# Kernel tuning notes

Hardware: AMD Instinct MI355X
Metric: run time of the kernel (lower is better)

## Reference

```python
import jax, jax.numpy as jnp
import numpy as np

N_PE = 100000   # num 'pe' nodes
N_R = 100000    # num 'router' nodes
E = 600000      # edges per relation
D_IN = 64       # input feature dim per node type
H = 128         # hidden_channels
G = 64          # graphs in batch


def setup_inputs() -> dict:
    key = jax.random.key(0)
    ks = jax.random.split(key, 20)
    inp = {}
    inp["x_pe"] = jax.random.normal(ks[0], (N_PE, D_IN), jnp.float32)
    inp["x_r"] = jax.random.normal(ks[1], (N_R, D_IN), jnp.float32)
    # edge_index per relation: row0 = src node ids, row1 = dst node ids
    inp["ei_per"] = jax.random.randint(ks[2], (2, E), 0, N_PE, jnp.int32)   # pe -> router
    inp["ei_rpe"] = jax.random.randint(ks[3], (2, E), 0, N_R, jnp.int32)    # router -> pe
    inp["ei_rr"] = jax.random.randint(ks[4], (2, E), 0, N_R, jnp.int32)     # router -> router
    inp["batch_pe"] = jnp.sort(jax.random.randint(ks[5], (N_PE,), 0, G, jnp.int32))
    inp["batch_r"] = jnp.sort(jax.random.randint(ks[6], (N_R,), 0, G, jnp.int32))
    # GraphConv params, relation axis ordered [pe->router, router->pe, router->router]
    s1 = 1.0 / np.sqrt(D_IN)
    s2 = 1.0 / np.sqrt(H)
    inp["Wrel1"] = jax.random.normal(ks[7], (3, D_IN, H), jnp.float32) * s1
    inp["brel1"] = jnp.zeros((3, H), jnp.float32)
    inp["Wroot1"] = jax.random.normal(ks[8], (3, D_IN, H), jnp.float32) * s1
    inp["Wrel23"] = jax.random.normal(ks[9], (2, 3, H, H), jnp.float32) * s2
    inp["brel23"] = jnp.zeros((2, 3, H), jnp.float32)
    inp["Wroot23"] = jax.random.normal(ks[10], (2, 3, H, H), jnp.float32) * s2
    # per-node-type MLP heads, type axis ordered [pe, router]
    inp["mlp_W1"] = jax.random.normal(ks[11], (2, H, 5), jnp.float32) * s2
    inp["mlp_b1"] = jnp.zeros((2, 5), jnp.float32)
    inp["mlp_W2"] = jax.random.normal(ks[12], (2, 5, 1), jnp.float32) * (1.0 / np.sqrt(5.0))
    inp["mlp_b2"] = jnp.zeros((2, 1), jnp.float32)
    inp["out_W"] = jax.random.normal(ks[13], (2, 1), jnp.float32) * (1.0 / np.sqrt(2.0))
    inp["out_b"] = jnp.zeros((1,), jnp.float32)
    return inp


def _hetero_graphconv(x_pe, x_r, ei_per, ei_rpe, ei_rr, Wrel, brel, Wroot):
    # GraphConv: lin_rel(scatter_add(x_src)) + lin_root(x_dst); to_hetero sums per dst type.
    agg_r_from_pe = jax.ops.segment_sum(x_pe[ei_per[0]], ei_per[1], num_segments=N_R)
    agg_pe_from_r = jax.ops.segment_sum(x_r[ei_rpe[0]], ei_rpe[1], num_segments=N_PE)
    agg_r_from_r = jax.ops.segment_sum(x_r[ei_rr[0]], ei_rr[1], num_segments=N_R)
    o_pe = agg_pe_from_r @ Wrel[1] + brel[1] + x_pe @ Wroot[1]
    o_r = (agg_r_from_pe @ Wrel[0] + brel[0] + x_r @ Wroot[0]) \
        + (agg_r_from_r @ Wrel[2] + brel[2] + x_r @ Wroot[2])
    return o_pe, o_r


def reference(x_pe, x_r, ei_per, ei_rpe, ei_rr, batch_pe, batch_r,
              Wrel1, brel1, Wroot1, Wrel23, brel23, Wroot23,
              mlp_W1, mlp_b1, mlp_W2, mlp_b2, out_W, out_b):
    h_pe, h_r = _hetero_graphconv(x_pe, x_r, ei_per, ei_rpe, ei_rr, Wrel1, brel1, Wroot1)
    h_pe, h_r = jax.nn.relu(h_pe), jax.nn.relu(h_r)
    h_pe, h_r = _hetero_graphconv(h_pe, h_r, ei_per, ei_rpe, ei_rr, Wrel23[0], brel23[0], Wroot23[0])
    h_pe, h_r = jax.nn.relu(h_pe), jax.nn.relu(h_r)
    h_pe, h_r = _hetero_graphconv(h_pe, h_r, ei_per, ei_rpe, ei_rr, Wrel23[1], brel23[1], Wroot23[1])
    gm_pe = jax.ops.segment_max(h_pe, batch_pe, num_segments=G)  # [G, H]
    gm_r = jax.ops.segment_max(h_r, batch_r, num_segments=G)
    def mlp(x, W1, b1, W2, b2):
        return jax.nn.relu(x @ W1 + b1) @ W2 + b2
    o_pe = mlp(gm_pe, mlp_W1[0], mlp_b1[0], mlp_W2[0], mlp_b2[0])  # [G, 1]
    o_r = mlp(gm_r, mlp_W1[1], mlp_b1[1], mlp_W2[1], mlp_b2[1])
    cat = jnp.concatenate([o_pe, o_r], axis=1)  # [G, 2]
    return cat @ out_W + out_b  # [G, 1]
```

## Files before the change

### kernel.cpp

```cpp
#include <hip/hip_runtime.h>
#include <cstddef>
#include <cstdint>

#define DIN 64
#define HID 128
#define NBKMAX 256
#define EPB 2048

typedef _Float16 half4v __attribute__((ext_vector_type(4)));
typedef _Float16 half8v __attribute__((ext_vector_type(8)));
typedef float f32x16 __attribute__((ext_vector_type(16)));

__device__ __forceinline__ unsigned encf(float f) {
    unsigned b = __float_as_uint(f);
    return (b & 0x80000000u) ? ~b : (b | 0x80000000u);
}
__device__ __forceinline__ float decf(unsigned u) {
    unsigned b = (u & 0x80000000u) ? (u & 0x7FFFFFFFu) : ~u;
    return __uint_as_float(b);
}

__global__ void conv_x2_k(const float* s0, _Float16* d0, int n40,
                          const float* s1, _Float16* d1, int n41) {
    int r = blockIdx.y;
    const float* s = r == 0 ? s0 : s1;
    _Float16* d = r == 0 ? d0 : d1;
    int n4 = r == 0 ? n40 : n41;
    int i = blockIdx.x * 256 + threadIdx.x;
    if (i >= n4) return;
    float4 v = *reinterpret_cast<const float4*>(&s[i * 4]);
    half4v h;
    h.x = (_Float16)v.x; h.y = (_Float16)v.y; h.z = (_Float16)v.z; h.w = (_Float16)v.w;
    *reinterpret_cast<half4v*>(&d[i * 4]) = h;
}

struct CW { const float* src; const float* src2; _Float16* dst; int K; int total; };
__global__ __launch_bounds__(256) void prep_k(
    CW c0, CW c1, CW c2, CW c3, CW c4, CW c5, CW c6, CW c7,
    const int* e0, const int* e1, const int* e2, int E,
    int* hc0, int* hc1, int* hc2,
    const int* bpe, int npe, int* spe,
    const int* brr, int nrr, int* srr, int G) {
    int y = blockIdx.y;
    if (y < 8) {
        CW J;
        switch (y) {
            case 0: J = c0; break; case 1: J = c1; break; case 2: J = c2; break;
            case 3: J = c3; break; case 4: J = c4; break; case 5: J = c5; break;
            case 6: J = c6; break; default: J = c7; break;
        }
        int i = blockIdx.x * 256 + threadIdx.x;
        if (i >= J.total) return;
        int m = i / (J.K * HID);
        int rem = i % (J.K * HID);
        int k = rem / HID;
        int col = rem % HID;
        float v = J.src[i];
        if (J.src2) v += J.src2[i];
        J.dst[(size_t)m * HID * J.K + (size_t)col * J.K + k] = (_Float16)v;
    } else if (y < 11) {
        int r = y - 8;
        const int* ei = r == 0 ? e0 : (r == 1 ? e1 : e2);
        int* cnt = r == 0 ? hc0 : (r == 1 ? hc1 : hc2);
        __shared__ int sc[NBKMAX];
        int t = threadIdx.x;
        sc[t] = 0;
        __syncthreads();
        int base = blockIdx.x * EPB;
        if (base >= E) return;
        int n = min(EPB, E - base);
        for (int i = t; i < n; i += 256)
            atomicAdd(&sc[(unsigned)ei[E + base + i] >> 9], 1);
        __syncthreads();
        if (sc[t]) atomicAdd(&cnt[t], sc[t]);
    } else {
        int r = blockIdx.x;
        if (r >= 2) return;
        const int* batch = r == 0 ? bpe : brr;
        int n = r == 0 ? npe : nrr;
        int* starts = r == 0 ? spe : srr;
        int g = threadIdx.x;
        if (g > G) return;
        int lo = 0, hi = n;
        while (lo < hi) {
            int mid = (lo + hi) >> 1;
            if (batch[mid] < g) lo = mid + 1; else hi = mid;
        }
        starts[g] = lo;
    }
}

__global__ __launch_bounds__(256) void bscan_k(int* c0, int* bb0, int* cu0, int* rp0, int n0,
                                               int* c1, int* bb1, int* cu1, int* rp1, int n1,
                                               int* c2, int* bb2, int* cu2, int* rp2, int n2,
                                               int E) {
    __shared__ int sh[256];
    int t = threadIdx.x;
    for (int r = 0; r < 3; ++r) {
        int* cnt = r == 0 ? c0 : (r == 1 ? c1 : c2);
        int* bb  = r == 0 ? bb0 : (r == 1 ? bb1 : bb2);
        int* cu  = r == 0 ? cu0 : (r == 1 ? cu1 : cu2);
        int* rp  = r == 0 ? rp0 : (r == 1 ? rp1 : rp2);
        int N    = r == 0 ? n0 : (r == 1 ? n1 : n2);
        int v = cnt[t];
        sh[t] = v;
        __syncthreads();
        for (int off = 1; off < 256; off <<= 1) {
            int val = (t >= off) ? sh[t - off] : 0;
            __syncthreads();
            sh[t] += val;
            __syncthreads();
        }
        int ex = sh[t] - v;
        bb[t] = ex;
        cu[t] = ex;
        if (t == 255) bb[256] = sh[255];
        if (t == 0) rp[N] = E;
        __syncthreads();
    }
}

__global__ __launch_bounds__(256) void bin_k(const int* e0, const int* e1, const int* e2, int E,
                                             int* cu0, int* cu1, int* cu2,
                                             unsigned* t0, unsigned* t1, unsigned* t2) {
    int r = blockIdx.y;
    const int* ei = r == 0 ? e0 : (r == 1 ? e1 : e2);
    int* gcur = r == 0 ? cu0 : (r == 1 ? cu1 : cu2);
    unsigned* temp = r == 0 ? t0 : (r == 1 ? t1 : t2);
    __shared__ unsigned pk[EPB];
    __shared__ unsigned short bkb[EPB];
    __shared__ int cnt[NBKMAX];
    __shared__ int scn[NBKMAX];
    __shared__ int rb[NBKMAX];
    int t = threadIdx.x;
    int base = blockIdx.x * EPB;
    int n = min(EPB, E - base);
    cnt[t] = 0;
    __syncthreads();
    for (int i = t; i < n; i += 256)
        atomicAdd(&cnt[(unsigned)ei[E + base + i] >> 9], 1);
    __syncthreads();
    {
        int v = cnt[t];
        scn[t] = v;
        __syncthreads();
        for (int off = 1; off < 256; off <<= 1) {
            int val = (t >= off) ? scn[t - off] : 0;
            __syncthreads();
            scn[t] += val;
            __syncthreads();
        }
        int ex = scn[t] - v;
        __syncthreads();
        scn[t] = ex;
    }
    {
        int c = cnt[t];
        rb[t] = c ? atomicAdd(&gcur[t], c) : 0;
        cnt[t] = 0;
    }
    __syncthreads();
    for (int i = t; i < n; i += 256) {
        int s = ei[base + i];
        int d = ei[E + base + i];
        int b = (unsigned)d >> 9;
        int slot = scn[b] + atomicAdd(&cnt[b], 1);
        pk[slot] = ((unsigned)s << 9) | (unsigned)(d & 511);
        bkb[slot] = (unsigned short)b;
    }
    __syncthreads();
    for (int i = t; i < n; i += 256) {
        int b = bkb[i];
        temp[rb[b] + (i - scn[b])] = pk[i];
    }
}

__global__ __launch_bounds__(256) void bcsr_k(const unsigned* t0, const unsigned* t1, const unsigned* t2,
                                              const int* bb0, const int* bb1, const int* bb2,
                                              int* rp0, int* rp1, int* rp2,
                                              int* a0, int* a1, int* a2,
                                              int n0, int n1, int n2) {
    int r = blockIdx.y;
    const unsigned* temp = r == 0 ? t0 : (r == 1 ? t1 : t2);
    const int* bb = r == 0 ? bb0 : (r == 1 ? bb1 : bb2);
    int* rp = r == 0 ? rp0 : (r == 1 ? rp1 : rp2);
    int* adj = r == 0 ? a0 : (r == 1 ? a1 : a2);
    int N = r == 0 ? n0 : (r == 1 ? n1 : n2);
    int b = blockIdx.x;
    int lo = bb[b], hi = bb[b + 1];
    __shared__ int cnt[512];
    __shared__ int sh[256];
    int t = threadIdx.x;
    cnt[t] = 0; cnt[t + 256] = 0;
    __syncthreads();
    for (int i = lo + t; i < hi; i += 256)
        atomicAdd(&cnt[temp[i] & 511], 1);
    __syncthreads();
    int c0 = cnt[2 * t], c1 = cnt[2 * t + 1];
    sh[t] = c0 + c1;
    __syncthreads();
    for (int off = 1; off < 256; off <<= 1) {
        int v = (t >= off) ? sh[t - off] : 0;
        __syncthreads();
        sh[t] += v;
        __syncthreads();
    }
    int pairExcl = sh[t] - (c0 + c1);
    __syncthreads();
    int e0x = lo + pairExcl;
    int e1x = e0x + c0;
    cnt[2 * t] = e0x;
    cnt[2 * t + 1] = e1x;
    int nodeBase = b * 512;
    if (nodeBase + 2 * t < N) rp[nodeBase + 2 * t] = e0x;
    if (nodeBase + 2 * t + 1 < N) rp[nodeBase + 2 * t + 1] = e1x;
    __syncthreads();
    for (int i = lo + t; i < hi; i += 256) {
        unsigned p = temp[i];
        int pos = atomicAdd(&cnt[p & 511], 1);
        adj[pos] = p >> 9;
    }
}

struct AJob { const _Float16* X; const int* rp; const int* adj; _Float16* AGG; int N; int gb; };
template <int D>
__global__ __launch_bounds__(256) void gather3_k(AJob a0, AJob a1, AJob a2) {
    int b = blockIdx.x;
    AJob J;
    if (b < a0.gb) { J = a0; }
    else if (b < a0.gb + a1.gb) { J = a1; b -= a0.gb; }
    else { J = a2; b -= a0.gb + a1.gb; }
    constexpr int TPN = D / 8;
    constexpr int NPB = 256 / TPN;
    int node = b * NPB + threadIdx.x / TPN;
    int glane = threadIdx.x % TPN;
    if (node >= J.N) return;
    int a = J.rp[node], e1 = J.rp[node + 1];
    float acc[8] = {0.f, 0.f, 0.f, 0.f, 0.f, 0.f, 0.f, 0.f};
    for (int base = a; base < e1; base += TPN) {
        int idx = base + glane;
        int myAdj = (idx < e1) ? J.adj[idx] : 0;
        int cnt = min(TPN, e1 - base);
        int j = 0;
        for (; j + 4 <= cnt; j += 4) {
            int s0 = __shfl(myAdj, j, TPN);
            int s1 = __shfl(myAdj, j + 1, TPN);
            int s2 = __shfl(myAdj, j + 2, TPN);
            int s3 = __shfl(myAdj, j + 3, TPN);
            half8v v0 = *reinterpret_cast<const half8v*>(&J.X[(size_t)s0 * D + glane * 8]);
            half8v v1 = *reinterpret_cast<const half8v*>(&J.X[(size_t)s1 * D + glane * 8]);
            half8v v2 = *reinterpret_cast<const half8v*>(&J.X[(size_t)s2 * D + glane * 8]);
            half8v v3 = *reinterpret_cast<const half8v*>(&J.X[(size_t)s3 * D + glane * 8]);
#pragma unroll
            for (int i = 0; i < 8; ++i)
                acc[i] += (float)v0[i] + (float)v1[i] + (float)v2[i] + (float)v3[i];
        }
        for (; j < cnt; ++j) {
            int s0 = __shfl(myAdj, j, TPN);
            half8v v0 = *reinterpret_cast<const half8v*>(&J.X[(size_t)s0 * D + glane * 8]);
#pragma unroll
            for (int i = 0; i < 8; ++i) acc[i] += (float)v0[i];
        }
    }
    half8v o;
#pragma unroll
    for (int i = 0; i < 8; ++i) o[i] = (_Float16)acc[i];
    *reinterpret_cast<half8v*>(&J.AGG[(size_t)node * D + glane * 8]) = o;
}

struct GJob {
    const _Float16* A0; const _Float16* A1; const _Float16* A2;
    const _Float16* W0; const _Float16* W1; const _Float16* W2;
    const float* b0; const float* b1;
    _Float16* O;
    int N; int total; int gb;
};

template <bool RELU>
__global__ __launch_bounds__(256) void gemm2_k(GJob j0, GJob j1, int K, int lg) {
    const bool second = ((int)blockIdx.x >= j0.gb);
    const GJob J = second ? j1 : j0;
    const int bx = blockIdx.x - (second ? j0.gb : 0);
    __shared__ _Float16 Alds[128 * 64];
    __shared__ _Float16 Wlds[128 * 64];
    const int tid = threadIdx.x;
    const int lane = tid & 63;
    const int w = tid >> 6;
    const int wr = w & 1, wc = w >> 1;
    const int rowBase = bx * 128;

    f32x16 acc[2][2];
#pragma unroll
    for (int r = 0; r < 2; ++r)
#pragma unroll
        for (int c = 0; c < 2; ++c)
#pragma unroll
            for (int q = 0; q < 16; ++q) acc[r][c][q] = 0.0f;

    const _Float16* Ap[3] = {J.A0, J.A1, J.A2};

    const int row = tid & 127;
    const int kh = (tid >> 7) * 32;
    const int gr = rowBase + row;
    const bool rowOK = (gr < J.N);
    int offS[4];
#pragma unroll
    for (int j = 0; j < 4; ++j) {
        int t = (kh >> 4) + (j >> 1);
        int k8 = j & 1;
        offS[j] = (((row >> 5) * 4 + t) * 64 + (row & 31) + 32 * k8) * 8;
    }

    const int total = J.total;
    const int cmask = (1 << lg) - 1;

    auto ldA = [&](int c, half8v h[4]) {
        int s = c >> lg;
        int k0 = (c & cmask) * 64;
        half8v z = {};
        h[0] = z; h[1] = z; h[2] = z; h[3] = z;
        if (rowOK) {
            const _Float16* p = Ap[s] + (size_t)gr * K + k0 + kh;
#pragma unroll
            for (int j = 0; j < 4; ++j) h[j] = *reinterpret_cast<const half8v*>(p + j * 8);
        }
    };
    auto ldW = [&](int c, half8v h[4]) {
        int s = c >> lg;
        int k0 = (c & cmask) * 64;
        const _Float16* __restrict__ Wt = (s == 0) ? J.W0 : (s == 1 ? J.W1 : J.W2);
        const _Float16* p = Wt + (size_t)row * K + k0 + kh;
#pragma unroll
        for (int j = 0; j < 4; ++j) h[j] = *reinterpret_cast<const half8v*>(p + j * 8);
    };

    half8v ra[4], rw[4];
    ldA(0, ra); ldW(0, rw);
#pragma unroll
    for (int j = 0; j < 4; ++j) {
        *reinterpret_cast<half8v*>(&Alds[offS[j]]) = ra[j];
        *reinterpret_cast<half8v*>(&Wlds[offS[j]]) = rw[j];
    }
    __syncthreads();

    for (int c = 0; c < total; ++c) {
        const bool more = (c + 1 < total);
        if (more) { ldA(c + 1, ra); ldW(c + 1, rw); }
#pragma unroll
        for (int t = 0; t < 4; ++t) {
            half8v av[2], wv[2];
#pragma unroll
            for (int r = 0; r < 2; ++r)
                av[r] = *reinterpret_cast<const half8v*>(&Alds[(((wr * 2 + r) * 4 + t) * 64 + lane) * 8]);
#pragma unroll
            for (int cc = 0; cc < 2; ++cc)
                wv[cc] = *reinterpret_cast<const half8v*>(&Wlds[(((wc * 2 + cc) * 4 + t) * 64 + lane) * 8]);
#pragma unroll
            for (int r = 0; r < 2; ++r)
#pragma unroll
                for (int cc = 0; cc < 2; ++cc)
                    acc[r][cc] = __builtin_amdgcn_mfma_f32_32x32x16_f16(wv[cc], av[r], acc[r][cc], 0, 0, 0);
        }
        __syncthreads();
        if (more) {
#pragma unroll
            for (int j = 0; j < 4; ++j) {
                *reinterpret_cast<half8v*>(&Alds[offS[j]]) = ra[j];
                *reinterpret_cast<half8v*>(&Wlds[offS[j]]) = rw[j];
            }
            __syncthreads();
        }
    }

    const int half_ = lane >> 5;
#pragma unroll
    for (int r = 0; r < 2; ++r) {
        int node = rowBase + (wr * 2 + r) * 32 + (lane & 31);
        bool ok = (node < J.N);
        _Float16* orow = J.O + (size_t)node * HID;
#pragma unroll
        for (int cc = 0; cc < 2; ++cc) {
            int fbase = wc * 64 + cc * 32;
#pragma unroll
            for (int g = 0; g < 4; ++g) {
                int fmine = fbase + g * 8 + 4 * half_;
                float4 bv = *reinterpret_cast<const float4*>(&J.b0[fmine]);
                if (J.b1) {
                    float4 b2v = *reinterpret_cast<const float4*>(&J.b1[fmine]);
                    bv.x += b2v.x; bv.y += b2v.y; bv.z += b2v.z; bv.w += b2v.w;
                }
                union { half4v h; int i[2]; } m, p;
#pragma unroll
                for (int i = 0; i < 4; ++i) {
                    float v = acc[r][cc][g * 4 + i] + ((const float*)&bv)[i];
                    if (RELU) v = fmaxf(v, 0.f);
                    m.h[i] = (_Float16)v;
                }
                p.i[0] = __shfl_xor(m.i[0], 32);
                p.i[1] = __shfl_xor(m.i[1], 32);
                half4v lo = half_ ? p.h : m.h;
                half4v hi = half_ ? m.h : p.h;
                half8v outv;
#pragma unroll
                for (int i = 0; i < 4; ++i) { outv[i] = lo[i]; outv[4 + i] = hi[i]; }
                if (ok && ((g & 1) == half_))
                    *reinterpret_cast<half8v*>(&orow[fbase + g * 8]) = outv;
            }
        }
    }
}

__global__ __launch_bounds__(128) void seg_max2_k(const _Float16* H0, const int* st0, unsigned* g0,
                                                  const _Float16* H1, const int* st1, unsigned* g1) {
    int z = blockIdx.z;
    const _Float16* Hf = z == 0 ? H0 : H1;
    const int* starts = z == 0 ? st0 : st1;
    unsigned* gmU = z == 0 ? g0 : g1;
    int g = blockIdx.x;
    int sub = blockIdx.y;
    int SUB = gridDim.y;
    int f = threadIdx.x;
    int s0 = starts[g], s1 = starts[g + 1];
    int len = s1 - s0;
    if (len <= 0) return;
    int chunk = (len + SUB - 1) / SUB;
    int a = s0 + sub * chunk;
    int b = min(a + chunk, s1);
    if (a >= b) return;
    float m = -__builtin_huge_valf();
    for (int n = a; n < b; ++n) m = fmaxf(m, (float)Hf[(size_t)n * HID + f]);
    atomicMax(&gmU[g * HID + f], encf(m));
}

__global__ void head_k(const unsigned* __restrict__ gmU_pe, const unsigned* __restrict__ gmU_r,
                       const float* __restrict__ W1, const float* __restrict__ b1,
                       const float* __restrict__ W2, const float* __restrict__ b2,
                       const float* __restrict__ oW, const float* __restrict__ ob,
                       float* __restrict__ out, int G) {
    int g = threadIdx.x;
    if (g >= G) return;
    float vals[2];
#pragma unroll
    for (int t = 0; t < 2; ++t) {
        const unsigned* gm = t ? gmU_r : gmU_pe;
        float z[5];
#pragma unroll
        for (int j = 0; j < 5; ++j) z[j] = b1[t * 5 + j];
        for (int f = 0; f < HID; ++f) {
            float x = decf(gm[g * HID + f]);
#pragma unroll
            for (int j = 0; j < 5; ++j) z[j] = fmaf(x, W1[t * HID * 5 + f * 5 + j], z[j]);
        }
        float o = b2[t];
#pragma unroll
        for (int j = 0; j < 5; ++j) o = fmaf(fmaxf(z[j], 0.f), W2[t * 5 + j], o);
        vals[t] = o;
    }
    out[g] = vals[0] * oW[0] + vals[1] * oW[1] + ob[0];
}

extern "C" void kernel_launch(void* const* d_in, const int* in_sizes, int n_in,
                              void* d_out, int out_size, void* d_ws, size_t ws_size,
                              hipStream_t stream) {
    const float* x_pe    = (const float*)d_in[0];
    const float* x_r     = (const float*)d_in[1];
    const int* ei_per    = (const int*)d_in[2];
    const int* ei_rpe    = (const int*)d_in[3];
    const int* ei_rr     = (const int*)d_in[4];
    const int* batch_pe  = (const int*)d_in[5];
    const int* batch_r   = (const int*)d_in[6];
    const float* Wrel1   = (const float*)d_in[7];
    const float* brel1   = (const float*)d_in[8];
    const float* Wroot1  = (const float*)d_in[9];
    const float* Wrel23  = (const float*)d_in[10];
    const float* brel23  = (const float*)d_in[11];
    const float* Wroot23 = (const float*)d_in[12];
    const float* mlp_W1  = (const float*)d_in[13];
    const float* mlp_b1  = (const float*)d_in[14];
    const float* mlp_W2  = (const float*)d_in[15];
    const float* mlp_b2  = (const float*)d_in[16];
    const float* out_W   = (const float*)d_in[17];
    const float* out_b   = (const float*)d_in[18];
    float* out = (float*)d_out;

    const int N_PE = in_sizes[0] / DIN;
    const int N_R  = in_sizes[1] / DIN;
    const int E    = in_sizes[2] / 2;
    const int G    = out_size;
    const int NMAX = (N_PE > N_R) ? N_PE : N_R;
    const size_t SZM = (size_t)NMAX * HID;

    _Float16* H1 = (_Float16*)d_ws;
    _Float16* H2 = H1 + SZM;
    _Float16* H3 = H2 + SZM;
    _Float16* H4 = H3 + SZM;
    _Float16* H5 = H4 + SZM;
    _Float16* xh_pe = H5 + SZM;
    _Float16* xh_r  = xh_pe + (size_t)N_PE * DIN;
    _Float16* wt_rel1    = xh_r + (size_t)N_R * DIN;
    _Float16* wt_root1pe = wt_rel1 + 3 * DIN * HID;
    _Float16* wt_wsum1   = wt_root1pe + DIN * HID;
    _Float16* wt_rel23   = wt_wsum1 + DIN * HID;
    _Float16* wt_root_l2 = wt_rel23 + 6 * HID * HID;
    _Float16* wt_root_l3 = wt_root_l2 + HID * HID;
    _Float16* wt_wsum2   = wt_root_l3 + HID * HID;
    _Float16* wt_wsum3   = wt_wsum2 + HID * HID;
    unsigned* gmU_pe = (unsigned*)(wt_wsum3 + HID * HID);
    unsigned* gmU_r  = gmU_pe + G * HID;
    int* bktCnt = (int*)(gmU_r + G * HID);
    int* starts_pe = bktCnt + 3 * NBKMAX;
    int* starts_r  = starts_pe + (G + 1);
    int* bb     = starts_r + (G + 1);
    int* gcur   = bb + 3 * (NBKMAX + 1);
    int* csr    = gcur + 3 * NBKMAX;
    const size_t relstride = (size_t)(NMAX + 1) + 2 * (size_t)E + 16;

    int* rp[3]; int* adjp[3]; unsigned* tmp[3];
    const int Nds[3] = {N_R, N_PE, N_R};
    for (int r = 0; r < 3; ++r) {
        int* rowptr = csr + (size_t)r * relstride;
        rp[r] = rowptr;
        adjp[r] = rowptr + (Nds[r] + 1);
        tmp[r] = (unsigned*)(adjp[r] + E);
    }

    const int gpe = (N_PE + 127) / 128, grr = (N_R + 127) / 128;
    const int eb = (E + EPB - 1) / EPB;

    hipMemsetAsync(gmU_pe, 0, (2 * (size_t)G * HID + 3 * NBKMAX) * sizeof(int), stream);
    {
        int n40 = N_PE * DIN / 4, n41 = N_R * DIN / 4;
        int nmax = n40 > n41 ? n40 : n41;
        dim3 g((nmax + 255) / 256, 2);
        conv_x2_k<<<g, 256, 0, stream>>>(x_pe, xh_pe, n40, x_r, xh_r, n41);
    }
    {
        CW c0{Wrel1, nullptr, wt_rel1, DIN, 3 * DIN * HID};
        CW c1{Wroot1 + 1 * DIN * HID, nullptr, wt_root1pe, DIN, DIN * HID};
        CW c2{Wroot1, Wroot1 + 2 * DIN * HID, wt_wsum1, DIN, DIN * HID};
        CW c3{Wrel23, nullptr, wt_rel23, HID, 6 * HID * HID};
        CW c4{Wroot23 + 1 * HID * HID, nullptr, wt_root_l2, HID, HID * HID};
        CW c5{Wroot23 + 4 * HID * HID, nullptr, wt_root_l3, HID, HID * HID};
        CW c6{Wroot23, Wroot23 + 2 * HID * HID, wt_wsum2, HID, HID * HID};
        CW c7{Wroot23 + 3 * HID * HID, Wroot23 + 5 * HID * HID, wt_wsum3, HID, HID * HID};
        int gx = (6 * HID * HID + 255) / 256;
        if (eb > gx) gx = eb;
        dim3 g(gx, 12);
        prep_k<<<g, 256, 0, stream>>>(c0, c1, c2, c3, c4, c5, c6, c7,
                                      ei_per, ei_rpe, ei_rr, E,
                                      bktCnt, bktCnt + NBKMAX, bktCnt + 2 * NBKMAX,
                                      batch_pe, N_PE, starts_pe,
                                      batch_r, N_R, starts_r, G);
    }
    {
        bscan_k<<<1, 256, 0, stream>>>(
            bktCnt, bb, gcur, rp[0], Nds[0],
            bktCnt + NBKMAX, bb + (NBKMAX + 1), gcur + NBKMAX, rp[1], Nds[1],
            bktCnt + 2 * NBKMAX, bb + 2 * (NBKMAX + 1), gcur + 2 * NBKMAX, rp[2], Nds[2], E);
        dim3 gh(eb, 3);
        bin_k<<<gh, 256, 0, stream>>>(ei_per, ei_rpe, ei_rr, E,
                                      gcur, gcur + NBKMAX, gcur + 2 * NBKMAX,
                                      tmp[0], tmp[1], tmp[2]);
        dim3 gc(NBKMAX, 3);
        bcsr_k<<<gc, 256, 0, stream>>>(tmp[0], tmp[1], tmp[2],
                                       bb, bb + (NBKMAX + 1), bb + 2 * (NBKMAX + 1),
                                       rp[0], rp[1], rp[2],
                                       adjp[0], adjp[1], adjp[2],
                                       Nds[0], Nds[1], Nds[2]);
    }

    {
        AJob a0{xh_r, rp[1], adjp[1], H1, N_PE, (N_PE + 31) / 32};
        AJob a1{xh_pe, rp[0], adjp[0], H2, N_R, (N_R + 31) / 32};
        AJob a2{xh_r, rp[2], adjp[2], H3, N_R, (N_R + 31) / 32};
        gather3_k<DIN><<<a0.gb + a1.gb + a2.gb, 256, 0, stream>>>(a0, a1, a2);
        GJob jp{H1, xh_pe, nullptr,
                wt_rel1 + 1 * DIN * HID, wt_root1pe, nullptr,
                brel1 + HID, nullptr, H4, N_PE, 2, gpe};
        GJob jr{H2, H3, xh_r,
                wt_rel1, wt_rel1 + 2 * DIN * HID, wt_wsum1,
                brel1, brel1 + 2 * HID, H5, N_R, 3, grr};
        gemm2_k<true><<<gpe + grr, 256, 0, stream>>>(jp, jr, DIN, 0);
    }
    {
        AJob a0{H5, rp[1], adjp[1], H1, N_PE, (N_PE + 15) / 16};
        AJob a1{H4, rp[0], adjp[0], H2, N_R, (N_R + 15) / 16};
        AJob a2{H5, rp[2], adjp[2], H3, N_R, (N_R + 15) / 16};
        gather3_k<HID><<<a0.gb + a1.gb + a2.gb, 256, 0, stream>>>(a0, a1, a2);
        GJob jp{H1, H4, nullptr,
                wt_rel23 + 1 * HID * HID, wt_root_l2, nullptr,
                brel23 + HID, nullptr, H1, N_PE, 2 * 2, gpe};
        GJob jr{H2, H3, H5,
                wt_rel23, wt_rel23 + 2 * HID * HID, wt_wsum2,
                brel23, brel23 + 2 * HID, H2, N_R, 3 * 2, grr};
        gemm2_k<true><<<gpe + grr, 256, 0, stream>>>(jp, jr, HID, 1);
    }
    {
        AJob a0{H2, rp[1], adjp[1], H3, N_PE, (N_PE + 15) / 16};
        AJob a1{H1, rp[0], adjp[0], H4, N_R, (N_R + 15) / 16};
        AJob a2{H2, rp[2], adjp[2], H5, N_R, (N_R + 15) / 16};
        gather3_k<HID><<<a0.gb + a1.gb + a2.gb, 256, 0, stream>>>(a0, a1, a2);
        GJob jp{H3, H1, nullptr,
                wt_rel23 + 4 * HID * HID, wt_root_l3, nullptr,
                brel23 + 4 * HID, nullptr, H3, N_PE, 2 * 2, gpe};
        GJob jr{H4, H5, H2,
                wt_rel23 + 3 * HID * HID, wt_rel23 + 5 * HID * HID, wt_wsum3,
                brel23 + 3 * HID, brel23 + 5 * HID, H4, N_R, 3 * 2, grr};
        gemm2_k<false><<<gpe + grr, 256, 0, stream>>>(jp, jr, HID, 1);
    }

    dim3 gs(G, 16, 2);
    seg_max2_k<<<gs, 128, 0, stream>>>(H3, starts_pe, gmU_pe, H4, starts_r, gmU_r);
    head_k<<<1, 64, 0, stream>>>(gmU_pe, gmU_r, mlp_W1, mlp_b1, mlp_W2, mlp_b2, out_W, out_b, out, G);
}
```

Measured before the change: 590.0 us.

## Double-buffer GEMM tiles via direct global-to-LDS loads with XOR swizzle

Rewrites the staging of the fused dual-job GEMM kernel. Tiles now go straight from global memory into LDS with global_load_lds instead of passing through registers, and the LDS buffers are doubled so the next K-chunk loads while the current one feeds MFMA. Each chunk ends with a single waitcnt+barrier instead of two syncthreads. An XOR swizzle on the 16-byte column groups is meant to avoid LDS bank conflicts on the fragment reads. The per-row bounds check on A is dropped, so the last partial row block may read past N unless the buffers are padded. LDS use also doubles, which may reduce occupancy.

New measurement: 547.9 us. 1.08x faster.

```diff
diff --git a/kernel.cpp b/kernel.cpp
--- a/kernel.cpp
+++ b/kernel.cpp
@@ -281,8 +281,8 @@
     const bool second = ((int)blockIdx.x >= j0.gb);
     const GJob J = second ? j1 : j0;
     const int bx = blockIdx.x - (second ? j0.gb : 0);
-    __shared__ _Float16 Alds[128 * 64];
-    __shared__ _Float16 Wlds[128 * 64];
+    __shared__ _Float16 Alds[2][128 * 64];
+    __shared__ _Float16 Wlds[2][128 * 64];
     const int tid = threadIdx.x;
     const int lane = tid & 63;
     const int w = tid >> 6;
@@ -298,78 +298,74 @@
             for (int q = 0; q < 16; ++q) acc[r][c][q] = 0.0f;
 
     const _Float16* Ap[3] = {J.A0, J.A1, J.A2};
-
-    const int row = tid & 127;
-    const int kh = (tid >> 7) * 32;
-    const int gr = rowBase + row;
-    const bool rowOK = (gr < J.N);
-    int offS[4];
-#pragma unroll
-    for (int j = 0; j < 4; ++j) {
-        int t = (kh >> 4) + (j >> 1);
-        int k8 = j & 1;
-        offS[j] = (((row >> 5) * 4 + t) * 64 + (row & 31) + 32 * k8) * 8;
+    const _Float16* Wp[3] = {J.W0, J.W1, J.W2};
+
+    int srow[4];
+    int soff[4];
+    int ldsoff[4];
+#pragma unroll
+    for (int i = 0; i < 4; ++i) {
+        int r_ = (w * 4 + i) * 8 + (lane >> 3);
+        srow[i] = r_;
+        soff[i] = ((lane & 7) ^ (r_ & 7)) << 4;
+        ldsoff[i] = (w * 4 + i) << 10;
     }
 
     const int total = J.total;
     const int cmask = (1 << lg) - 1;
 
-    auto ldA = [&](int c, half8v h[4]) {
-        int s = c >> lg;
-        int k0 = (c & cmask) * 64;
-        half8v z = {};
-        h[0] = z; h[1] = z; h[2] = z; h[3] = z;
-        if (rowOK) {
-            const _Float16* p = Ap[s] + (size_t)gr * K + k0 + kh;
-#pragma unroll
-            for (int j = 0; j < 4; ++j) h[j] = *reinterpret_cast<const half8v*>(p + j * 8);
+    auto stage = [&](int c, int buf) {
+        const int s = c >> lg;
+        const int k0b = (c & cmask) << 7;
+        const char* Ab = (const char*)Ap[s];
+        const char* Wb = (const char*)Wp[s];
+        char* al = (char*)&Alds[buf][0];
+        char* wl = (char*)&Wlds[buf][0];
+#pragma unroll
+        for (int i = 0; i < 4; ++i) {
+            const char* ga = Ab + ((size_t)(rowBase + srow[i]) * K) * 2 + k0b + soff[i];
+            const char* gw = Wb + ((size_t)srow[i] * K) * 2 + k0b + soff[i];
+            __builtin_amdgcn_global_load_lds(
+                (const __attribute__((address_space(1))) void*)ga,
+                (__attribute__((address_space(3))) void*)(al + ldsoff[i]), 16, 0, 0);
+            __builtin_amdgcn_global_load_lds(
+                (const __attribute__((address_space(1))) void*)gw,
+                (__attribute__((address_space(3))) void*)(wl + ldsoff[i]), 16, 0, 0);
         }
     };
-    auto ldW = [&](int c, half8v h[4]) {
-        int s = c >> lg;
-        int k0 = (c & cmask) * 64;
-        const _Float16* __restrict__ Wt = (s == 0) ? J.W0 : (s == 1 ? J.W1 : J.W2);
-        const _Float16* p = Wt + (size_t)row * K + k0 + kh;
-#pragma unroll
-        for (int j = 0; j < 4; ++j) h[j] = *reinterpret_cast<const half8v*>(p + j * 8);
-    };
-
-    half8v ra[4], rw[4];
-    ldA(0, ra); ldW(0, rw);
-#pragma unroll
-    for (int j = 0; j < 4; ++j) {
-        *reinterpret_cast<half8v*>(&Alds[offS[j]]) = ra[j];
-        *reinterpret_cast<half8v*>(&Wlds[offS[j]]) = rw[j];
-    }
-    __syncthreads();
+
+    stage(0, 0);
+    asm volatile("s_waitcnt vmcnt(0)\n\ts_barrier" ::: "memory");
+
+    const int rA0 = wr * 64 + (lane & 31);
+    const int cW0 = wc * 64 + (lane & 31);
+    const int ghi = lane >> 5;
 
     for (int c = 0; c < total; ++c) {
-        const bool more = (c + 1 < total);
-        if (more) { ldA(c + 1, ra); ldW(c + 1, rw); }
+        if (c + 1 < total) stage(c + 1, (c + 1) & 1);
+        const _Float16* al = &Alds[c & 1][0];
+        const _Float16* wl = &Wlds[c & 1][0];
 #pragma unroll
         for (int t = 0; t < 4; ++t) {
+            const int g = 2 * t + ghi;
             half8v av[2], wv[2];
 #pragma unroll
-            for (int r = 0; r < 2; ++r)
-                av[r] = *reinterpret_cast<const half8v*>(&Alds[(((wr * 2 + r) * 4 + t) * 64 + lane) * 8]);
-#pragma unroll
-            for (int cc = 0; cc < 2; ++cc)
-                wv[cc] = *reinterpret_cast<const half8v*>(&Wlds[(((wc * 2 + cc) * 4 + t) * 64 + lane) * 8]);
+            for (int r = 0; r < 2; ++r) {
+                const int row = rA0 + r * 32;
+                av[r] = *reinterpret_cast<const half8v*>(al + ((row * 8 + (g ^ (row & 7))) << 3));
+            }
+#pragma unroll
+            for (int cc = 0; cc < 2; ++cc) {
+                const int col = cW0 + cc * 32;
+                wv[cc] = *reinterpret_cast<const half8v*>(wl + ((col * 8 + (g ^ (col & 7))) << 3));
+            }
 #pragma unroll
             for (int r = 0; r < 2; ++r)
 #pragma unroll
                 for (int cc = 0; cc < 2; ++cc)
                     acc[r][cc] = __builtin_amdgcn_mfma_f32_32x32x16_f16(wv[cc], av[r], acc[r][cc], 0, 0, 0);
         }
-        __syncthreads();
-        if (more) {
-#pragma unroll
-            for (int j = 0; j < 4; ++j) {
-                *reinterpret_cast<half8v*>(&Alds[offS[j]]) = ra[j];
-                *reinterpret_cast<half8v*>(&Wlds[offS[j]]) = rw[j];
-            }
-            __syncthreads();
-        }
+        asm volatile("s_waitcnt vmcnt(0)\n\ts_barrier" ::: "memory");
     }
 
     const int half_ = lane >> 5;
```
